# Optimization experiments

Hardware: AMD Instinct MI355X
Metric: run time of the kernel (lower is better)

Reference implementation:

```python
import jax, jax.numpy as jnp
import numpy as np

DIM = 1024  # dim_model

def setup_inputs() -> dict:
    key = jax.random.key(0)
    ks = jax.random.split(key, 7)
    B, S, E = 4, 2048, 2 * DIM
    scale = 1.0 / np.sqrt(DIM)
    inputs = jax.random.normal(ks[0], (B, S, E), dtype=jnp.float32)
    Wq = jax.random.normal(ks[1], (DIM, DIM), dtype=jnp.float32) * scale
    bq = jax.random.normal(ks[2], (DIM,), dtype=jnp.float32) * 0.01
    Wk = jax.random.normal(ks[3], (DIM, DIM), dtype=jnp.float32) * scale
    bk = jax.random.normal(ks[4], (DIM,), dtype=jnp.float32) * 0.01
    Wv = jax.random.normal(ks[5], (DIM, DIM), dtype=jnp.float32) * scale
    bv = jax.random.normal(ks[6], (DIM,), dtype=jnp.float32) * 0.01
    return {"inputs": inputs, "Wq": Wq, "bq": bq, "Wk": Wk, "bk": bk, "Wv": Wv, "bv": bv}

def reference(inputs, Wq, bq, Wk, bk, Wv, bv):
    E = inputs.shape[-1]
    d = E // 2  # == dim_model
    vision_repr = inputs[:, :, :d]
    text_repr = inputs[:, :, d:]
    # torch nn.Linear: y = x @ W^T + b
    query = jnp.einsum('bsd,ed->bse', vision_repr, Wq) + bq
    key = jnp.einsum('bsd,ed->bse', text_repr, Wk) + bk
    value = jnp.einsum('bsd,ed->bse', text_repr, Wv) + bv
    scores = jnp.einsum('bqd,bkd->bqk', query, key) / jnp.sqrt(jnp.float32(d))
    attn = jax.nn.softmax(scores, axis=-1)  # [B, S, S]
    cross_attended_vision = jnp.einsum('bqk,bkd->bqd', attn, value)
    cross_attended_text = jnp.einsum('bqk,bqd->bkd', attn, vision_repr)
    return (cross_attended_vision, cross_attended_text)
```

## Files before the change

### kernel.cpp

```cpp
#include <hip/hip_runtime.h>

typedef unsigned short u16;
typedef unsigned int u32;
typedef __bf16 bf16x8 __attribute__((ext_vector_type(8)));
typedef float f32x4 __attribute__((ext_vector_type(4)));
typedef u16 u16x4 __attribute__((ext_vector_type(4)));
typedef u16 u16x8 __attribute__((ext_vector_type(8)));

__device__ __forceinline__ float b2f(u16 u) {
  union { float f; u32 i; } x; x.i = ((u32)u) << 16; return x.f;
}
__device__ __forceinline__ u16 f2b(float f) {
  union { float f; u32 i; } x; x.f = f;
  u32 r = (x.i + 0x7fffu + ((x.i >> 16) & 1u)) >> 16;
  return (u16)r;
}

__device__ __forceinline__ void gload16(const void* g, void* l) {
  __builtin_amdgcn_global_load_lds(
      (const __attribute__((address_space(1))) void*)g,
      (__attribute__((address_space(3))) void*)l, 16, 0, 0);
}


__global__ void convert_split(const float* __restrict__ in,
                              u16* __restrict__ vis, u16* __restrict__ txt) {
  size_t i = ((size_t)blockIdx.x * 256 + threadIdx.x) * 4;
  f32x4 v = *reinterpret_cast<const f32x4*>(in + i);
  size_t row = i >> 11;
  int col = (int)(i & 2047);
  u16x4 o = { f2b(v[0]), f2b(v[1]), f2b(v[2]), f2b(v[3]) };
  u16* dst = (col < 1024) ? (vis + row * 1024 + col)
                          : (txt + row * 1024 + (col - 1024));
  *reinterpret_cast<u16x4*>(dst) = o;
}

__global__ void convert_bf16(const float* __restrict__ in, u16* __restrict__ out) {
  size_t i = ((size_t)blockIdx.x * 256 + threadIdx.x) * 4;
  f32x4 v = *reinterpret_cast<const f32x4*>(in + i);
  u16x4 o = { f2b(v[0]), f2b(v[1]), f2b(v[2]), f2b(v[3]) };
  *reinterpret_cast<u16x4*>(out + i) = o;
}

__global__ void transpose_vision(const float* __restrict__ in, u16* __restrict__ out) {
  __shared__ float tile[64][65];
  const float* src = in + (size_t)blockIdx.z * (2048u * 2048u);
  u16* dst = out + (size_t)blockIdx.z * (1024u * 2048u);
  const int t = threadIdx.x;
  const int s0 = blockIdx.y * 64, d0 = blockIdx.x * 64;
#pragma unroll
  for (int p = 0; p < 16; ++p) {
    int idx = p * 256 + t; int r = idx >> 6, c = idx & 63;
    tile[r][c] = src[(size_t)(s0 + r) * 2048 + d0 + c];
  }
  __syncthreads();
#pragma unroll
  for (int p = 0; p < 16; ++p) {
    int idx = p * 256 + t; int r = idx >> 6, c = idx & 63;
    dst[(size_t)(d0 + r) * 2048 + s0 + c] = f2b(tile[c][r]);
  }
}

__global__ void transpose_bf16(const u16* __restrict__ in, u16* __restrict__ out,
                               int rows, int cols, long inB, long outB) {
  __shared__ u16 tile[64][65];
  const u16* src = in + (size_t)blockIdx.z * inB;
  u16* dst = out + (size_t)blockIdx.z * outB;
  const int t = threadIdx.x;
  const int r0 = blockIdx.y * 64, c0 = blockIdx.x * 64;
#pragma unroll
  for (int p = 0; p < 16; ++p) {
    int idx = p * 256 + t; int r = idx >> 6, c = idx & 63;
    tile[r][c] = src[(size_t)(r0 + r) * cols + c0 + c];
  }
  __syncthreads();
#pragma unroll
  for (int p = 0; p < 16; ++p) {
    int idx = p * 256 + t; int r = idx >> 6, c = idx & 63;
    dst[(size_t)(c0 + r) * rows + r0 + c] = tile[c][r];
  }
}

__launch_bounds__(256)
__global__ void softmax_kernel(u16* __restrict__ S) {
  __shared__ float red[8];
  u16* p = S + (size_t)blockIdx.x * 2048;
  const int t = threadIdx.x;
  u16x8 u = *reinterpret_cast<const u16x8*>(p + t * 8);
  float v[8];
#pragma unroll
  for (int j = 0; j < 8; ++j) v[j] = b2f(u[j]);
  float mx = v[0];
#pragma unroll
  for (int j = 1; j < 8; ++j) mx = fmaxf(mx, v[j]);
#pragma unroll
  for (int off = 32; off; off >>= 1) mx = fmaxf(mx, __shfl_xor(mx, off));
  if ((t & 63) == 0) red[t >> 6] = mx;
  __syncthreads();
  mx = fmaxf(fmaxf(red[0], red[1]), fmaxf(red[2], red[3]));
  float e[8], s = 0.f;
#pragma unroll
  for (int j = 0; j < 8; ++j) { e[j] = __expf(v[j] - mx); s += e[j]; }
#pragma unroll
  for (int off = 32; off; off >>= 1) s += __shfl_xor(s, off);
  if ((t & 63) == 0) red[4 + (t >> 6)] = s;
  __syncthreads();
  s = red[4] + red[5] + red[6] + red[7];
  const float inv = 1.0f / s;
  u16x8 o;
#pragma unroll
  for (int j = 0; j < 8; ++j) o[j] = f2b(e[j] * inv);
  *reinterpret_cast<u16x8*>(p + t * 8) = o;
}

template<int MODE>
__launch_bounds__(256)
__global__ void gemm_nt(const u16* __restrict__ A, const u16* __restrict__ B,
                        const float* __restrict__ bias, void* __restrict__ Cout,
                        int K, int lda, int ldb, int ldc,
                        long sA, long sB, long sC, float scale) {
  __shared__ u16 lds[2][2][128 * 32];
  const int t = threadIdx.x;
  const size_t z = blockIdx.z;
  A += z * (size_t)sA;
  B += z * (size_t)sB;
  const int bm = blockIdx.y, bn = blockIdx.x;
  const int lane = t & 63;
  const int wave = t >> 6;
  const int wr = (wave >> 1) << 6, wc = (wave & 1) << 6;
  const int fr = lane & 15, kh = lane >> 4;

  const int rA = bm * 128 + (t >> 2);
  const int rB = bn * 128 + (t >> 2);
  const int ck = (t & 3) << 3;

  f32x4 acc[4][4];
  const f32x4 zero = {0.f, 0.f, 0.f, 0.f};
#pragma unroll
  for (int i = 0; i < 4; ++i)
#pragma unroll
    for (int j = 0; j < 4; ++j) acc[i][j] = zero;

  const int nk = K >> 5;

  auto STAGE = [&](int b, int k0) {
#pragma unroll
    for (int p = 0; p < 2; ++p) {
      gload16(A + (size_t)(rA + (p << 6)) * lda + k0 + ck,
              (char*)&lds[b][0][0] + t * 16 + p * 4096);
      gload16(B + (size_t)(rB + (p << 6)) * ldb + k0 + ck,
              (char*)&lds[b][1][0] + t * 16 + p * 4096);
    }
  };

  STAGE(0, 0);
  __syncthreads();
  int cur = 0;
  for (int kt = 0; kt < nk; ++kt) {
    if (kt + 1 < nk) STAGE(cur ^ 1, (kt + 1) << 5);
    bf16x8 af[4], bg[4];
    const u16* la = &lds[cur][0][0];
    const u16* lb = &lds[cur][1][0];
#pragma unroll
    for (int i = 0; i < 4; ++i)
      af[i] = *reinterpret_cast<const bf16x8*>(la + (wr + i * 16 + fr) * 32 + kh * 8);
#pragma unroll
    for (int j = 0; j < 4; ++j)
      bg[j] = *reinterpret_cast<const bf16x8*>(lb + (wc + j * 16 + fr) * 32 + kh * 8);
#pragma unroll
    for (int i = 0; i < 4; ++i)
#pragma unroll
      for (int j = 0; j < 4; ++j)
        acc[i][j] = __builtin_amdgcn_mfma_f32_16x16x32_bf16(af[i], bg[j], acc[i][j], 0, 0, 0);
    __syncthreads();
    cur ^= 1;
  }

  const int m0 = bm * 128 + wr + kh * 4;
  const int n0 = bn * 128 + wc + fr;
#pragma unroll
  for (int i = 0; i < 4; ++i) {
#pragma unroll
    for (int j = 0; j < 4; ++j) {
      const int n = n0 + j * 16;
      const float bb = (MODE == 0 && bias) ? bias[n] : 0.f;
#pragma unroll
      for (int r = 0; r < 4; ++r) {
        const int m = m0 + i * 16 + r;
        float v = acc[i][j][r] * scale + bb;
        if (MODE == 0)
          ((u16*)Cout)[z * (size_t)sC + (size_t)m * ldc + n] = f2b(v);
        else
          ((float*)Cout)[z * (size_t)sC + (size_t)m * ldc + n] = v;
      }
    }
  }
}

extern "C" void kernel_launch(void* const* d_in, const int* in_sizes, int n_in,
                              void* d_out, int out_size, void* d_ws, size_t ws_size,
                              hipStream_t stream) {
  const float* inp = (const float*)d_in[0];
  const float* Wq  = (const float*)d_in[1];
  const float* bq  = (const float*)d_in[2];
  const float* Wk  = (const float*)d_in[3];
  const float* bk  = (const float*)d_in[4];
  const float* Wv  = (const float*)d_in[5];
  const float* bv  = (const float*)d_in[6];
  float* out = (float*)d_out;
  char* ws = (char*)d_ws;

  u16* visB  = (u16*)(ws + 0);
  u16* textB = (u16*)(ws + 16777216);
  u16* Vtmp  = (u16*)(ws + 0);
  u16* Sattn = (u16*)(ws + 0);
  u16* visT  = (u16*)(ws + 33554432);
  u16* WqB   = (u16*)(ws + 50331648);
  u16* WkB   = (u16*)(ws + 52428800);
  u16* WvB   = (u16*)(ws + 54525952);
  u16* Qb    = (u16*)(ws + 56623104);
  u16* Kb    = (u16*)(ws + 73400320);
  u16* attnT = (u16*)(ws + 56623104);
  u16* Vt    = (u16*)(ws + 90177536);

  convert_split<<<16384, 256, 0, stream>>>(inp, visB, textB);
  convert_bf16<<<1024, 256, 0, stream>>>(Wq, WqB);
  convert_bf16<<<1024, 256, 0, stream>>>(Wk, WkB);
  convert_bf16<<<1024, 256, 0, stream>>>(Wv, WvB);
  transpose_vision<<<dim3(16, 32, 4), 256, 0, stream>>>(inp, visT);

  gemm_nt<0><<<dim3(8, 64, 1), 256, 0, stream>>>(visB,  WqB, bq, Qb,   1024, 1024, 1024, 1024, 0, 0, 0, 1.f);
  gemm_nt<0><<<dim3(8, 64, 1), 256, 0, stream>>>(textB, WkB, bk, Kb,   1024, 1024, 1024, 1024, 0, 0, 0, 1.f);
  gemm_nt<0><<<dim3(8, 64, 1), 256, 0, stream>>>(textB, WvB, bv, Vtmp, 1024, 1024, 1024, 1024, 0, 0, 0, 1.f);

  transpose_bf16<<<dim3(16, 32, 4), 256, 0, stream>>>(Vtmp, Vt, 2048, 1024, 2048L * 1024, 1024L * 2048);

  gemm_nt<0><<<dim3(16, 16, 4), 256, 0, stream>>>(Qb, Kb, nullptr, Sattn, 1024, 1024, 1024, 2048,
                                                  2097152, 2097152, 4194304, 0.03125f);
  softmax_kernel<<<8192, 256, 0, stream>>>(Sattn);

  transpose_bf16<<<dim3(32, 32, 4), 256, 0, stream>>>(Sattn, attnT, 2048, 2048, 4194304L, 4194304L);

  gemm_nt<2><<<dim3(8, 16, 4), 256, 0, stream>>>(Sattn, Vt, nullptr, out, 2048, 2048, 2048, 1024,
                                                 4194304, 2097152, 2097152, 1.f);
  gemm_nt<2><<<dim3(8, 16, 4), 256, 0, stream>>>(attnT, visT, nullptr, out + 8388608, 2048, 2048, 2048, 1024,
                                                 4194304, 2097152, 2097152, 1.f);
}
```

Before: 406.0 us.

## Replace 128x128 GEMM with 256x256 pipelined swizzled kernel and batch launches

```diff
diff --git a/kernel.cpp b/kernel.cpp
--- a/kernel.cpp
+++ b/kernel.cpp
@@ -113,85 +113,180 @@
   *reinterpret_cast<u16x8*>(p + t * 8) = o;
 }
 
-template<int MODE>
-__launch_bounds__(256)
-__global__ void gemm_nt(const u16* __restrict__ A, const u16* __restrict__ B,
-                        const float* __restrict__ bias, void* __restrict__ Cout,
-                        int K, int lda, int ldb, int ldc,
-                        long sA, long sB, long sC, float scale) {
-  __shared__ u16 lds[2][2][128 * 32];
+
+struct GArgs {
+  const u16* A[8]; const u16* B[8]; const float* bias[8]; void* C[8];
+  int K, lda, ldb, ldc; float scale; int obf16;
+};
+
+#define FENCE() asm volatile("" ::: "memory")
+#define BARF()  { FENCE(); __builtin_amdgcn_s_barrier(); FENCE(); }
+#define LGKM0() { asm volatile("s_waitcnt lgkmcnt(0)" ::: "memory"); __builtin_amdgcn_sched_barrier(0); }
+#define LGKM8() asm volatile("s_waitcnt lgkmcnt(8)" ::: "memory")
+#define VMC4()  asm volatile("s_waitcnt vmcnt(4)" ::: "memory")
+#define PRIO1() __builtin_amdgcn_s_setprio(1)
+#define PRIO0() { __builtin_amdgcn_s_setprio(0); __builtin_amdgcn_sched_barrier(0); }
+
+__launch_bounds__(512, 2)
+__global__ void gemm256(GArgs args) {
+  __shared__ u16 lds[65536];
+  char* L = (char*)lds;
   const int t = threadIdx.x;
-  const size_t z = blockIdx.z;
-  A += z * (size_t)sA;
-  B += z * (size_t)sB;
+  const int z = blockIdx.z;
+  const u16* A  = args.A[z];
+  const u16* Bm = args.B[z];
+  const int K = args.K, lda = args.lda, ldb = args.ldb, ldc = args.ldc;
   const int bm = blockIdx.y, bn = blockIdx.x;
-  const int lane = t & 63;
-  const int wave = t >> 6;
-  const int wr = (wave >> 1) << 6, wc = (wave & 1) << 6;
+  const int lane = t & 63, wave = t >> 6;
+  const int wr = (wave >> 2) * 128;
+  const int wc = (wave & 3) * 64;
   const int fr = lane & 15, kh = lane >> 4;
-
-  const int rA = bm * 128 + (t >> 2);
-  const int rB = bn * 128 + (t >> 2);
-  const int ck = (t & 3) << 3;
-
-  f32x4 acc[4][4];
+  const int sw = (fr & 7) << 4;
+  const u32 cK0 = (u32)((kh << 4) ^ sw);
+  const u32 cK1 = (u32)((64 | (kh << 4)) ^ sw);
+  const u32 offA = (u32)((wr ? 16384 : 0) + fr * 128);
+  const u32 offB = (u32)(32768 + ((wc & 128) ? 16384 : 0) + ((wc & 64) ? 8192 : 0) + fr * 128);
+  const int srow = t >> 3;
+  const int scol = ((((t & 7) << 4) ^ (((t >> 3) & 7) << 4)) >> 1);
+  const u32 sdst = (u32)(t * 16);
+  const u16* Ab = A  + (size_t)(bm * 256 + srow) * lda + scol;
+  const u16* Bb = Bm + (size_t)(bn * 256 + srow) * ldb + scol;
+
+  f32x4 acc[8][4];
   const f32x4 zero = {0.f, 0.f, 0.f, 0.f};
 #pragma unroll
-  for (int i = 0; i < 4; ++i)
-#pragma unroll
-    for (int j = 0; j < 4; ++j) acc[i][j] = zero;
-
-  const int nk = K >> 5;
-
-  auto STAGE = [&](int b, int k0) {
-#pragma unroll
-    for (int p = 0; p < 2; ++p) {
-      gload16(A + (size_t)(rA + (p << 6)) * lda + k0 + ck,
-              (char*)&lds[b][0][0] + t * 16 + p * 4096);
-      gload16(B + (size_t)(rB + (p << 6)) * ldb + k0 + ck,
-              (char*)&lds[b][1][0] + t * 16 + p * 4096);
-    }
-  };
-
-  STAGE(0, 0);
-  __syncthreads();
-  int cur = 0;
-  for (int kt = 0; kt < nk; ++kt) {
-    if (kt + 1 < nk) STAGE(cur ^ 1, (kt + 1) << 5);
-    bf16x8 af[4], bg[4];
-    const u16* la = &lds[cur][0][0];
-    const u16* lb = &lds[cur][1][0];
-#pragma unroll
-    for (int i = 0; i < 4; ++i)
-      af[i] = *reinterpret_cast<const bf16x8*>(la + (wr + i * 16 + fr) * 32 + kh * 8);
-#pragma unroll
-    for (int j = 0; j < 4; ++j)
-      bg[j] = *reinterpret_cast<const bf16x8*>(lb + (wc + j * 16 + fr) * 32 + kh * 8);
-#pragma unroll
-    for (int i = 0; i < 4; ++i)
-#pragma unroll
-      for (int j = 0; j < 4; ++j)
-        acc[i][j] = __builtin_amdgcn_mfma_f32_16x16x32_bf16(af[i], bg[j], acc[i][j], 0, 0, 0);
-    __syncthreads();
-    cur ^= 1;
-  }
-
-  const int m0 = bm * 128 + wr + kh * 4;
-  const int n0 = bn * 128 + wc + fr;
-#pragma unroll
-  for (int i = 0; i < 4; ++i) {
-#pragma unroll
-    for (int j = 0; j < 4; ++j) {
-      const int n = n0 + j * 16;
-      const float bb = (MODE == 0 && bias) ? bias[n] : 0.f;
-#pragma unroll
-      for (int r = 0; r < 4; ++r) {
-        const int m = m0 + i * 16 + r;
-        float v = acc[i][j][r] * scale + bb;
-        if (MODE == 0)
-          ((u16*)Cout)[z * (size_t)sC + (size_t)m * ldc + n] = f2b(v);
-        else
-          ((float*)Cout)[z * (size_t)sC + (size_t)m * ldc + n] = v;
+  for (int a = 0; a < 8; ++a)
+#pragma unroll
+    for (int n = 0; n < 4; ++n) acc[a][n] = zero;
+
+  bf16x8 af[4][2], bg0[2][2], bg1[2][2];
+
+  auto STAGE_A = [&](int bufOff, int half, int k0) {
+    const u16* s = Ab + (size_t)(half * 128) * lda + k0;
+    char* d = L + bufOff + half * 16384 + sdst;
+    gload16(s, d);
+    gload16(s + (size_t)64 * lda, d + 8192);
+  };
+  auto STAGE_B = [&](int bufOff, int half, int k0) {
+    const u16* s = Bb + (size_t)(half * 128) * ldb + k0;
+    char* d = L + bufOff + 32768 + half * 16384 + sdst;
+    gload16(s, d);
+    gload16(s + (size_t)64 * ldb, d + 8192);
+  };
+  auto LDA = [&](int bufOff, int h) {
+#pragma unroll
+    for (int mi = 0; mi < 4; ++mi) {
+      u32 base = (u32)bufOff + offA + (u32)(h * 8192 + mi * 2048);
+      af[mi][0] = *reinterpret_cast<const bf16x8*>(L + base + cK0);
+      af[mi][1] = *reinterpret_cast<const bf16x8*>(L + base + cK1);
+    }
+  };
+  auto LDB = [&](int bufOff, int g, bf16x8 (&bg)[2][2]) {
+#pragma unroll
+    for (int ni = 0; ni < 2; ++ni) {
+      u32 base = (u32)bufOff + offB + (u32)(g * 4096 + ni * 2048);
+      bg[ni][0] = *reinterpret_cast<const bf16x8*>(L + base + cK0);
+      bg[ni][1] = *reinterpret_cast<const bf16x8*>(L + base + cK1);
+    }
+  };
+  auto MF = [&](int h, int g, bf16x8 (&bg)[2][2]) {
+#pragma unroll
+    for (int mi = 0; mi < 4; ++mi)
+#pragma unroll
+      for (int ni = 0; ni < 2; ++ni)
+#pragma unroll
+        for (int kk = 0; kk < 2; ++kk)
+          acc[h * 4 + mi][g * 2 + ni] = __builtin_amdgcn_mfma_f32_16x16x32_bf16(
+              af[mi][kk], bg[ni][kk], acc[h * 4 + mi][g * 2 + ni], 0, 0, 0);
+  };
+
+  STAGE_A(0, 0, 0); STAGE_A(0, 1, 0); STAGE_B(0, 0, 0); STAGE_B(0, 1, 0);
+  STAGE_B(65536, 0, 64); STAGE_B(65536, 1, 64);
+  VMC4();
+  BARF();
+
+  const int nIter = K >> 7;
+  for (int it = 0; it < nIter; ++it) {
+    const int tt = it * 2;
+    const int k1 = (tt + 1) << 6;
+    int k2 = (tt + 2) << 6; if (k2 >= K) k2 = 0;
+    int k3 = (tt + 3) << 6; if (k3 >= K) k3 = 0;
+    LDA(0, 0); LDB(0, 0, bg0);
+    STAGE_A(65536, 0, k1);
+    LGKM8();
+    BARF(); LGKM0();
+    PRIO1(); MF(0, 0, bg0); PRIO0();
+    BARF();
+    LDB(0, 1, bg1);
+    STAGE_A(65536, 1, k1);
+    BARF(); LGKM0();
+    PRIO1(); MF(0, 1, bg1); PRIO0();
+    BARF();
+    LDA(0, 1);
+    STAGE_B(0, 0, k2);
+    BARF(); LGKM0();
+    PRIO1(); MF(1, 1, bg1); PRIO0();
+    BARF();
+    STAGE_B(0, 1, k2);
+    BARF();
+    PRIO1(); MF(1, 0, bg0); PRIO0();
+    VMC4();
+    BARF();
+    LDA(65536, 0); LDB(65536, 0, bg0);
+    STAGE_A(0, 0, k2);
+    LGKM8();
+    BARF(); LGKM0();
+    PRIO1(); MF(0, 0, bg0); PRIO0();
+    BARF();
+    LDB(65536, 1, bg1);
+    STAGE_A(0, 1, k2);
+    BARF(); LGKM0();
+    PRIO1(); MF(0, 1, bg1); PRIO0();
+    BARF();
+    LDA(65536, 1);
+    STAGE_B(65536, 0, k3);
+    BARF(); LGKM0();
+    PRIO1(); MF(1, 1, bg1); PRIO0();
+    BARF();
+    STAGE_B(65536, 1, k3);
+    BARF();
+    PRIO1(); MF(1, 0, bg0); PRIO0();
+    VMC4();
+    BARF();
+  }
+
+  const float scl = args.scale;
+  const float* bias = args.bias[z];
+  float bv[4];
+#pragma unroll
+  for (int ni = 0; ni < 4; ++ni) {
+    int n = bn * 256 + wc + ni * 16 + fr;
+    bv[ni] = bias ? bias[n] : 0.f;
+  }
+  if (args.obf16) {
+    u16* C = (u16*)args.C[z];
+#pragma unroll
+    for (int a = 0; a < 8; ++a) {
+      const int mb = bm * 256 + wr + (a >> 2) * 64 + (a & 3) * 16 + kh * 4;
+#pragma unroll
+      for (int ni = 0; ni < 4; ++ni) {
+        const int n = bn * 256 + wc + ni * 16 + fr;
+#pragma unroll
+        for (int r = 0; r < 4; ++r)
+          C[(size_t)(mb + r) * ldc + n] = f2b(acc[a][ni][r] * scl + bv[ni]);
+      }
+    }
+  } else {
+    float* C = (float*)args.C[z];
+#pragma unroll
+    for (int a = 0; a < 8; ++a) {
+      const int mb = bm * 256 + wr + (a >> 2) * 64 + (a & 3) * 16 + kh * 4;
+#pragma unroll
+      for (int ni = 0; ni < 4; ++ni) {
+        const int n = bn * 256 + wc + ni * 16 + fr;
+#pragma unroll
+        for (int r = 0; r < 4; ++r)
+          C[(size_t)(mb + r) * ldc + n] = acc[a][ni][r] * scl + bv[ni];
       }
     }
   }
@@ -229,20 +324,48 @@
   convert_bf16<<<1024, 256, 0, stream>>>(Wv, WvB);
   transpose_vision<<<dim3(16, 32, 4), 256, 0, stream>>>(inp, visT);
 
-  gemm_nt<0><<<dim3(8, 64, 1), 256, 0, stream>>>(visB,  WqB, bq, Qb,   1024, 1024, 1024, 1024, 0, 0, 0, 1.f);
-  gemm_nt<0><<<dim3(8, 64, 1), 256, 0, stream>>>(textB, WkB, bk, Kb,   1024, 1024, 1024, 1024, 0, 0, 0, 1.f);
-  gemm_nt<0><<<dim3(8, 64, 1), 256, 0, stream>>>(textB, WvB, bv, Vtmp, 1024, 1024, 1024, 1024, 0, 0, 0, 1.f);
+  {
+    GArgs g{};
+    g.A[0] = visB;  g.B[0] = WqB; g.bias[0] = bq; g.C[0] = Qb;
+    g.A[1] = textB; g.B[1] = WkB; g.bias[1] = bk; g.C[1] = Kb;
+    g.A[2] = textB; g.B[2] = WvB; g.bias[2] = bv; g.C[2] = Vtmp;
+    g.K = 1024; g.lda = 1024; g.ldb = 1024; g.ldc = 1024; g.scale = 1.f; g.obf16 = 1;
+    gemm256<<<dim3(4, 32, 3), 512, 0, stream>>>(g);
+  }
 
   transpose_bf16<<<dim3(16, 32, 4), 256, 0, stream>>>(Vtmp, Vt, 2048, 1024, 2048L * 1024, 1024L * 2048);
 
-  gemm_nt<0><<<dim3(16, 16, 4), 256, 0, stream>>>(Qb, Kb, nullptr, Sattn, 1024, 1024, 1024, 2048,
-                                                  2097152, 2097152, 4194304, 0.03125f);
+  {
+    GArgs g{};
+    for (int z = 0; z < 4; ++z) {
+      g.A[z] = Qb + (size_t)z * 2097152;
+      g.B[z] = Kb + (size_t)z * 2097152;
+      g.bias[z] = nullptr;
+      g.C[z] = Sattn + (size_t)z * 4194304;
+    }
+    g.K = 1024; g.lda = 1024; g.ldb = 1024; g.ldc = 2048; g.scale = 0.03125f; g.obf16 = 1;
+    gemm256<<<dim3(8, 8, 4), 512, 0, stream>>>(g);
+  }
+
   softmax_kernel<<<8192, 256, 0, stream>>>(Sattn);
 
   transpose_bf16<<<dim3(32, 32, 4), 256, 0, stream>>>(Sattn, attnT, 2048, 2048, 4194304L, 4194304L);
 
-  gemm_nt<2><<<dim3(8, 16, 4), 256, 0, stream>>>(Sattn, Vt, nullptr, out, 2048, 2048, 2048, 1024,
-                                                 4194304, 2097152, 2097152, 1.f);
-  gemm_nt<2><<<dim3(8, 16, 4), 256, 0, stream>>>(attnT, visT, nullptr, out + 8388608, 2048, 2048, 2048, 1024,
-                                                 4194304, 2097152, 2097152, 1.f);
-}
+  {
+    GArgs g{};
+    for (int z = 0; z < 4; ++z) {
+      g.A[z] = Sattn + (size_t)z * 4194304;
+      g.B[z] = Vt + (size_t)z * 2097152;
+      g.bias[z] = nullptr;
+      g.C[z] = out + (size_t)z * 2097152;
+    }
+    for (int z = 4; z < 8; ++z) {
+      g.A[z] = attnT + (size_t)(z - 4) * 4194304;
+      g.B[z] = visT + (size_t)(z - 4) * 2097152;
+      g.bias[z] = nullptr;
+      g.C[z] = out + 8388608 + (size_t)(z - 4) * 2097152;
+    }
+    g.K = 2048; g.lda = 2048; g.ldb = 2048; g.ldc = 1024; g.scale = 1.f; g.obf16 = 0;
+    gemm256<<<dim3(4, 8, 8), 512, 0, stream>>>(g);
+  }
+}
```

After: 338.1 us. 16.7% less time.
